# Optimization experiments

Hardware: AMD Instinct MI355X
Metric: run time of the kernel (lower is better)

The kernel has to match this reference:

```python
import jax, jax.numpy as jnp
import numpy as np

LR = 0.01        # memory update learning rate (init kwarg lr)
INIT_SCALE = 0.01
B, N, D = 8, 1024, 256


def setup_inputs() -> dict:
    key = jax.random.key(0)
    k1, k2, k3, k4, k5 = jax.random.split(key, 5)
    return {
        "sequence": jax.random.normal(k1, (B, N, D), dtype=jnp.float32),
        "targets": jax.random.normal(k2, (B, N, D), dtype=jnp.float32),
        "theta0": jax.random.normal(k3, (D, D), dtype=jnp.float32) * INIT_SCALE,
        "W_e": jax.random.normal(k4, (D, D), dtype=jnp.float32) * INIT_SCALE,
        "W_o": jax.random.normal(k5, (D, D), dtype=jnp.float32) * INIT_SCALE,
    }


def reference(sequence, targets, theta0, W_e, W_o):
    # process_sequence on (batch, n, d) with targets: theta is reset to theta0
    # for each batch element, then updated sequentially per token (delta rule).
    def step(theta, xt):
        x_t, tgt_t = xt                      # (d,), (d,)
        h = W_e @ x_t                        # encode: F.linear(x, W_e)
        pred = theta @ h                     # predict with current memory
        err = tgt_t - pred
        theta_new = theta + LR * jnp.outer(err, h)   # rank-1 fast-weight update
        out = W_o @ pred                     # output projection of PREDICTION
        return theta_new, out

    def per_batch(seq_b, tgt_b):             # (n, d), (n, d)
        _, outs = jax.lax.scan(step, theta0, (seq_b, tgt_b))
        return outs                          # (n, d)

    return jax.vmap(per_batch)(sequence, targets)   # (batch, n, d)
```

## Files before the change

kernel.cpp:

```cpp
#include <hip/hip_runtime.h>

#define LR_C 0.01f
#define NB 8
#define NTOK 1024
#define DD 256

#define DPP_ADD(x, ctrl) \
    ((x) + __int_as_float(__builtin_amdgcn_update_dpp( \
        0, __float_as_int(x), (ctrl), 0xF, 0xF, true)))

#define TBM 128
#define TBN 64
#define TBK 16

__global__ __launch_bounds__(256) void gemm_abt_kernel(
    const float* __restrict__ A, const float* __restrict__ B,
    float* __restrict__ C)
{
    __shared__ float As[TBK][TBM + 4];
    __shared__ float Bs[TBK][TBN + 4];
    const int t    = threadIdx.x;
    const int arow = t >> 1, ak = (t & 1) * 8;
    const int brow = t >> 2, bk = (t & 3) * 4;
    const int tx   = t & 15, ty = t >> 4;

    const float* Ap = A + (size_t)(blockIdx.x * TBM + arow) * DD + ak;
    const float* Bp = B + (size_t)(blockIdx.y * TBN + brow) * DD + bk;

    float4 acc[8];
    #pragma unroll
    for (int i = 0; i < 8; ++i) acc[i] = make_float4(0.f, 0.f, 0.f, 0.f);

    float4 a0 = *reinterpret_cast<const float4*>(Ap);
    float4 a1 = *reinterpret_cast<const float4*>(Ap + 4);
    float4 b0 = *reinterpret_cast<const float4*>(Bp);

    for (int k0 = 0; k0 < DD; k0 += TBK) {
        __syncthreads();
        As[ak + 0][arow] = a0.x; As[ak + 1][arow] = a0.y;
        As[ak + 2][arow] = a0.z; As[ak + 3][arow] = a0.w;
        As[ak + 4][arow] = a1.x; As[ak + 5][arow] = a1.y;
        As[ak + 6][arow] = a1.z; As[ak + 7][arow] = a1.w;
        Bs[bk + 0][brow] = b0.x; Bs[bk + 1][brow] = b0.y;
        Bs[bk + 2][brow] = b0.z; Bs[bk + 3][brow] = b0.w;
        __syncthreads();
        if (k0 + TBK < DD) {
            a0 = *reinterpret_cast<const float4*>(Ap + k0 + TBK);
            a1 = *reinterpret_cast<const float4*>(Ap + k0 + TBK + 4);
            b0 = *reinterpret_cast<const float4*>(Bp + k0 + TBK);
        }
        #pragma unroll
        for (int k = 0; k < TBK; ++k) {
            float4 av0 = *reinterpret_cast<const float4*>(&As[k][ty * 8]);
            float4 av1 = *reinterpret_cast<const float4*>(&As[k][ty * 8 + 4]);
            float4 bv  = *reinterpret_cast<const float4*>(&Bs[k][tx * 4]);
            float ar[8] = {av0.x, av0.y, av0.z, av0.w, av1.x, av1.y, av1.z, av1.w};
            #pragma unroll
            for (int i = 0; i < 8; ++i) {
                acc[i].x = fmaf(ar[i], bv.x, acc[i].x);
                acc[i].y = fmaf(ar[i], bv.y, acc[i].y);
                acc[i].z = fmaf(ar[i], bv.z, acc[i].z);
                acc[i].w = fmaf(ar[i], bv.w, acc[i].w);
            }
        }
    }
    #pragma unroll
    for (int i = 0; i < 8; ++i) {
        float* cp = C + (size_t)(blockIdx.x * TBM + ty * 8 + i) * DD
                      + blockIdx.y * TBN + tx * 4;
        *reinterpret_cast<float4*>(cp) = acc[i];
    }
}

#define PF 8

__global__ __launch_bounds__(64) void theta_scan_kernel(
    const float* __restrict__ H, const float* __restrict__ Tgt,
    const float* __restrict__ theta0, float* __restrict__ Pred)
{
    const int blk  = blockIdx.x;
    const int b    = blk >> 8;
    const int row  = blk & 255;
    const int lane = threadIdx.x;

    float4 th = *reinterpret_cast<const float4*>(
        theta0 + (size_t)row * DD + lane * 4);

    const float* Hb = H    + (size_t)b * NTOK * DD + lane * 4;
    const float* Tb = Tgt  + (size_t)b * NTOK * DD + row;
    float*       Pb = Pred + (size_t)b * NTOK * DD + row;

    float4 hp[PF]; float tp[PF];
    #pragma unroll
    for (int p = 0; p < PF; ++p) {
        hp[p] = *reinterpret_cast<const float4*>(Hb + (size_t)p * DD);
        tp[p] = Tb[(size_t)p * DD];
    }

    for (int t0 = 0; t0 < NTOK; t0 += PF) {
        float predv = 0.f;
        #pragma unroll
        for (int p = 0; p < PF; ++p) {
            const int t = t0 + p;
            const float4 h  = hp[p];
            const float  tg = tp[p];
            int tn = t + PF; if (tn > NTOK - 1) tn = NTOK - 1;
            hp[p] = *reinterpret_cast<const float4*>(Hb + (size_t)tn * DD);
            tp[p] = Tb[(size_t)tn * DD];

            float s = th.x * h.x;
            s = fmaf(th.y, h.y, s);
            s = fmaf(th.z, h.z, s);
            s = fmaf(th.w, h.w, s);
            s = DPP_ADD(s, 0xB1);
            s = DPP_ADD(s, 0x4E);
            s = DPP_ADD(s, 0x141);
            s = DPP_ADD(s, 0x140);
            s = DPP_ADD(s, 0x142);
            s = DPP_ADD(s, 0x143);
            const float stot = __int_as_float(
                __builtin_amdgcn_readlane(__float_as_int(s), 63));

            predv = (lane == p) ? stot : predv;

            const float e = LR_C * (tg - stot);
            th.x = fmaf(e, h.x, th.x);
            th.y = fmaf(e, h.y, th.y);
            th.z = fmaf(e, h.z, th.z);
            th.w = fmaf(e, h.w, th.w);
        }
        if (lane < PF) Pb[(size_t)(t0 + lane) * DD] = predv;
    }
}

extern "C" void kernel_launch(void* const* d_in, const int* in_sizes, int n_in,
                              void* d_out, int out_size, void* d_ws, size_t ws_size,
                              hipStream_t stream) {
    const float* seq    = (const float*)d_in[0];
    const float* tgt    = (const float*)d_in[1];
    const float* theta0 = (const float*)d_in[2];
    const float* W_e    = (const float*)d_in[3];
    const float* W_o    = (const float*)d_in[4];
    float* out = (float*)d_out;

    float* Hbuf = (float*)d_ws;
    float* Pbuf = Hbuf + (size_t)NB * NTOK * DD;

    dim3 ggrid(NB * NTOK / TBM, DD / TBN);

    gemm_abt_kernel<<<ggrid, 256, 0, stream>>>(seq, W_e, Hbuf);
    theta_scan_kernel<<<NB * 256, 64, 0, stream>>>(Hbuf, tgt, theta0, Pbuf);
    gemm_abt_kernel<<<ggrid, 256, 0, stream>>>(Pbuf, W_o, out);
}
```

Baseline: 228.5 us.

## Chunk the delta-rule scan using precomputed intra-chunk Gram matrices

```diff
diff --git a/kernel.cpp b/kernel.cpp
--- a/kernel.cpp
+++ b/kernel.cpp
@@ -4,12 +4,23 @@
 #define NB 8
 #define NTOK 1024
 #define DD 256
+#define CH 8
+#define NCHUNK (NTOK / CH)
 
 #define DPP_ADD(x, ctrl) \
     ((x) + __int_as_float(__builtin_amdgcn_update_dpp( \
         0, __float_as_int(x), (ctrl), 0xF, 0xF, true)))
 
-#define TBM 128
+#define REDUCE_ALL64(s) do { \
+    s = DPP_ADD(s, 0xB1); \
+    s = DPP_ADD(s, 0x4E); \
+    s = DPP_ADD(s, 0x141); \
+    s = DPP_ADD(s, 0x140); \
+    s += __shfl_xor(s, 16, 64); \
+    s += __shfl_xor(s, 32, 64); \
+} while (0)
+
+#define TBM 64
 #define TBN 64
 #define TBK 16
 
@@ -20,63 +31,130 @@
     __shared__ float As[TBK][TBM + 4];
     __shared__ float Bs[TBK][TBN + 4];
     const int t    = threadIdx.x;
-    const int arow = t >> 1, ak = (t & 1) * 8;
-    const int brow = t >> 2, bk = (t & 3) * 4;
+    const int lrow = t >> 2, lk = (t & 3) * 4;
     const int tx   = t & 15, ty = t >> 4;
 
-    const float* Ap = A + (size_t)(blockIdx.x * TBM + arow) * DD + ak;
-    const float* Bp = B + (size_t)(blockIdx.y * TBN + brow) * DD + bk;
-
-    float4 acc[8];
-    #pragma unroll
-    for (int i = 0; i < 8; ++i) acc[i] = make_float4(0.f, 0.f, 0.f, 0.f);
+    const float* Ap = A + (size_t)(blockIdx.x * TBM + lrow) * DD + lk;
+    const float* Bp = B + (size_t)(blockIdx.y * TBN + lrow) * DD + lk;
+
+    float4 acc[4];
+    #pragma unroll
+    for (int i = 0; i < 4; ++i) acc[i] = make_float4(0.f, 0.f, 0.f, 0.f);
 
     float4 a0 = *reinterpret_cast<const float4*>(Ap);
-    float4 a1 = *reinterpret_cast<const float4*>(Ap + 4);
     float4 b0 = *reinterpret_cast<const float4*>(Bp);
 
     for (int k0 = 0; k0 < DD; k0 += TBK) {
         __syncthreads();
-        As[ak + 0][arow] = a0.x; As[ak + 1][arow] = a0.y;
-        As[ak + 2][arow] = a0.z; As[ak + 3][arow] = a0.w;
-        As[ak + 4][arow] = a1.x; As[ak + 5][arow] = a1.y;
-        As[ak + 6][arow] = a1.z; As[ak + 7][arow] = a1.w;
-        Bs[bk + 0][brow] = b0.x; Bs[bk + 1][brow] = b0.y;
-        Bs[bk + 2][brow] = b0.z; Bs[bk + 3][brow] = b0.w;
+        As[lk + 0][lrow] = a0.x; As[lk + 1][lrow] = a0.y;
+        As[lk + 2][lrow] = a0.z; As[lk + 3][lrow] = a0.w;
+        Bs[lk + 0][lrow] = b0.x; Bs[lk + 1][lrow] = b0.y;
+        Bs[lk + 2][lrow] = b0.z; Bs[lk + 3][lrow] = b0.w;
         __syncthreads();
         if (k0 + TBK < DD) {
             a0 = *reinterpret_cast<const float4*>(Ap + k0 + TBK);
-            a1 = *reinterpret_cast<const float4*>(Ap + k0 + TBK + 4);
             b0 = *reinterpret_cast<const float4*>(Bp + k0 + TBK);
         }
         #pragma unroll
         for (int k = 0; k < TBK; ++k) {
-            float4 av0 = *reinterpret_cast<const float4*>(&As[k][ty * 8]);
-            float4 av1 = *reinterpret_cast<const float4*>(&As[k][ty * 8 + 4]);
-            float4 bv  = *reinterpret_cast<const float4*>(&Bs[k][tx * 4]);
-            float ar[8] = {av0.x, av0.y, av0.z, av0.w, av1.x, av1.y, av1.z, av1.w};
-            #pragma unroll
-            for (int i = 0; i < 8; ++i) {
-                acc[i].x = fmaf(ar[i], bv.x, acc[i].x);
-                acc[i].y = fmaf(ar[i], bv.y, acc[i].y);
-                acc[i].z = fmaf(ar[i], bv.z, acc[i].z);
-                acc[i].w = fmaf(ar[i], bv.w, acc[i].w);
-            }
+            float4 av = *reinterpret_cast<const float4*>(&As[k][ty * 4]);
+            float4 bv = *reinterpret_cast<const float4*>(&Bs[k][tx * 4]);
+            acc[0].x = fmaf(av.x, bv.x, acc[0].x); acc[0].y = fmaf(av.x, bv.y, acc[0].y);
+            acc[0].z = fmaf(av.x, bv.z, acc[0].z); acc[0].w = fmaf(av.x, bv.w, acc[0].w);
+            acc[1].x = fmaf(av.y, bv.x, acc[1].x); acc[1].y = fmaf(av.y, bv.y, acc[1].y);
+            acc[1].z = fmaf(av.y, bv.z, acc[1].z); acc[1].w = fmaf(av.y, bv.w, acc[1].w);
+            acc[2].x = fmaf(av.z, bv.x, acc[2].x); acc[2].y = fmaf(av.z, bv.y, acc[2].y);
+            acc[2].z = fmaf(av.z, bv.z, acc[2].z); acc[2].w = fmaf(av.z, bv.w, acc[2].w);
+            acc[3].x = fmaf(av.w, bv.x, acc[3].x); acc[3].y = fmaf(av.w, bv.y, acc[3].y);
+            acc[3].z = fmaf(av.w, bv.z, acc[3].z); acc[3].w = fmaf(av.w, bv.w, acc[3].w);
         }
     }
     #pragma unroll
-    for (int i = 0; i < 8; ++i) {
-        float* cp = C + (size_t)(blockIdx.x * TBM + ty * 8 + i) * DD
+    for (int i = 0; i < 4; ++i) {
+        float* cp = C + (size_t)(blockIdx.x * TBM + ty * 4 + i) * DD
                       + blockIdx.y * TBN + tx * 4;
         *reinterpret_cast<float4*>(cp) = acc[i];
     }
 }
 
-#define PF 8
+__global__ __launch_bounds__(64) void gram_kernel(
+    const float* __restrict__ H, float* __restrict__ Gram)
+{
+    const int blk  = blockIdx.x;
+    const int lane = threadIdx.x;
+    const float* Hc = H + (size_t)blk * CH * DD + lane * 4;
+
+    float4 h[CH];
+    #pragma unroll
+    for (int i = 0; i < CH; ++i)
+        h[i] = *reinterpret_cast<const float4*>(Hc + (size_t)i * DD);
+
+    float sel = 0.f;
+    #pragma unroll
+    for (int i = 1; i < CH; ++i) {
+        #pragma unroll
+        for (int j = 0; j < i; ++j) {
+            float s = h[j].x * h[i].x;
+            s = fmaf(h[j].y, h[i].y, s);
+            s = fmaf(h[j].z, h[i].z, s);
+            s = fmaf(h[j].w, h[i].w, s);
+            REDUCE_ALL64(s);
+            const int idx = i * (i - 1) / 2 + j;
+            sel = (lane == idx) ? s : sel;
+        }
+    }
+    if (lane < 28) Gram[(size_t)blk * 32 + lane] = sel;
+}
+
+#define STEP(HC, TC, CC, HN, TN, CN, ch) do { \
+    const int nc_ = ((ch) + 1 < NCHUNK) ? (ch) + 1 : NCHUNK - 1; \
+    const float* hsrc_ = Hb + (size_t)nc_ * CH * DD; \
+    const float* tsrc_ = Tb + (size_t)nc_ * CH * DD; \
+    const float* gsrc_ = Gb + nc_ * 32; \
+    _Pragma("unroll") \
+    for (int i_ = 0; i_ < CH; ++i_) { \
+        HN[i_] = *reinterpret_cast<const float4*>(hsrc_ + (size_t)i_ * DD); \
+        TN[i_] = LR_C * tsrc_[(size_t)i_ * DD]; \
+    } \
+    _Pragma("unroll") \
+    for (int q_ = 0; q_ < 28; ++q_) CN[q_] = gsrc_[q_]; \
+    float a_[CH]; \
+    _Pragma("unroll") \
+    for (int i_ = 0; i_ < CH; ++i_) { \
+        float s_ = HC[i_].x * th.x; \
+        s_ = fmaf(HC[i_].y, th.y, s_); \
+        s_ = fmaf(HC[i_].z, th.z, s_); \
+        s_ = fmaf(HC[i_].w, th.w, s_); \
+        REDUCE_ALL64(s_); \
+        a_[i_] = s_; \
+    } \
+    float e_[CH], p_[CH]; \
+    _Pragma("unroll") \
+    for (int i_ = 0; i_ < CH; ++i_) { \
+        float pv_ = a_[i_]; \
+        _Pragma("unroll") \
+        for (int j_ = 0; j_ < i_; ++j_) \
+            pv_ = fmaf(e_[j_], CC[i_ * (i_ - 1) / 2 + j_], pv_); \
+        p_[i_] = pv_; \
+        e_[i_] = fmaf(-LR_C, pv_, TC[i_]); \
+    } \
+    _Pragma("unroll") \
+    for (int j_ = 0; j_ < CH; ++j_) { \
+        th.x = fmaf(e_[j_], HC[j_].x, th.x); \
+        th.y = fmaf(e_[j_], HC[j_].y, th.y); \
+        th.z = fmaf(e_[j_], HC[j_].z, th.z); \
+        th.w = fmaf(e_[j_], HC[j_].w, th.w); \
+    } \
+    float sel_ = p_[0]; \
+    _Pragma("unroll") \
+    for (int i_ = 1; i_ < CH; ++i_) sel_ = (lane == i_) ? p_[i_] : sel_; \
+    if (lane < CH) Pb[(size_t)((ch) * CH + lane) * DD] = sel_; \
+} while (0)
 
 __global__ __launch_bounds__(64) void theta_scan_kernel(
     const float* __restrict__ H, const float* __restrict__ Tgt,
-    const float* __restrict__ theta0, float* __restrict__ Pred)
+    const float* __restrict__ theta0, const float* __restrict__ Gram,
+    float* __restrict__ Pred)
 {
     const int blk  = blockIdx.x;
     const int b    = blk >> 8;
@@ -88,48 +166,23 @@
 
     const float* Hb = H    + (size_t)b * NTOK * DD + lane * 4;
     const float* Tb = Tgt  + (size_t)b * NTOK * DD + row;
+    const float* Gb = Gram + (size_t)b * NCHUNK * 32;
     float*       Pb = Pred + (size_t)b * NTOK * DD + row;
 
-    float4 hp[PF]; float tp[PF];
-    #pragma unroll
-    for (int p = 0; p < PF; ++p) {
-        hp[p] = *reinterpret_cast<const float4*>(Hb + (size_t)p * DD);
-        tp[p] = Tb[(size_t)p * DD];
-    }
-
-    for (int t0 = 0; t0 < NTOK; t0 += PF) {
-        float predv = 0.f;
-        #pragma unroll
-        for (int p = 0; p < PF; ++p) {
-            const int t = t0 + p;
-            const float4 h  = hp[p];
-            const float  tg = tp[p];
-            int tn = t + PF; if (tn > NTOK - 1) tn = NTOK - 1;
-            hp[p] = *reinterpret_cast<const float4*>(Hb + (size_t)tn * DD);
-            tp[p] = Tb[(size_t)tn * DD];
-
-            float s = th.x * h.x;
-            s = fmaf(th.y, h.y, s);
-            s = fmaf(th.z, h.z, s);
-            s = fmaf(th.w, h.w, s);
-            s = DPP_ADD(s, 0xB1);
-            s = DPP_ADD(s, 0x4E);
-            s = DPP_ADD(s, 0x141);
-            s = DPP_ADD(s, 0x140);
-            s = DPP_ADD(s, 0x142);
-            s = DPP_ADD(s, 0x143);
-            const float stot = __int_as_float(
-                __builtin_amdgcn_readlane(__float_as_int(s), 63));
-
-            predv = (lane == p) ? stot : predv;
-
-            const float e = LR_C * (tg - stot);
-            th.x = fmaf(e, h.x, th.x);
-            th.y = fmaf(e, h.y, th.y);
-            th.z = fmaf(e, h.z, th.z);
-            th.w = fmaf(e, h.w, th.w);
-        }
-        if (lane < PF) Pb[(size_t)(t0 + lane) * DD] = predv;
+    float4 hA[CH]; float tA[CH], cA[28];
+    float4 hB[CH]; float tB[CH], cB[28];
+
+    #pragma unroll
+    for (int i = 0; i < CH; ++i) {
+        hA[i] = *reinterpret_cast<const float4*>(Hb + (size_t)i * DD);
+        tA[i] = LR_C * Tb[(size_t)i * DD];
+    }
+    #pragma unroll
+    for (int q = 0; q < 28; ++q) cA[q] = Gb[q];
+
+    for (int ch = 0; ch < NCHUNK; ch += 2) {
+        STEP(hA, tA, cA, hB, tB, cB, ch);
+        STEP(hB, tB, cB, hA, tA, cA, ch + 1);
     }
 }
 
@@ -145,10 +198,12 @@
 
     float* Hbuf = (float*)d_ws;
     float* Pbuf = Hbuf + (size_t)NB * NTOK * DD;
+    float* Cbuf = out;
 
     dim3 ggrid(NB * NTOK / TBM, DD / TBN);
 
     gemm_abt_kernel<<<ggrid, 256, 0, stream>>>(seq, W_e, Hbuf);
-    theta_scan_kernel<<<NB * 256, 64, 0, stream>>>(Hbuf, tgt, theta0, Pbuf);
+    gram_kernel<<<NB * NCHUNK, 64, 0, stream>>>(Hbuf, Cbuf);
+    theta_scan_kernel<<<NB * 256, 64, 0, stream>>>(Hbuf, tgt, theta0, Cbuf, Pbuf);
     gemm_abt_kernel<<<ggrid, 256, 0, stream>>>(Pbuf, W_o, out);
 }
```

Result: faster. 223.6 us (-2.1%).
